# Performance work log

Measured on AMD Instinct MI355X. Metric: run time of the kernel, lower is better.

Reference implementation:

```python
import jax, jax.numpy as jnp
import numpy as np

S, F, H, A, B = 11, 650, 1024, 47, 4096
NEG = -1e9  # stand-in for -inf in masked_fill; softmax weight becomes exactly 0 numerically


def _layernorm(x, g, b):
    m = x.mean(-1, keepdims=True)
    v = ((x - m) ** 2).mean(-1, keepdims=True)
    return (x - m) / jnp.sqrt(v + 1e-5) * g + b


def setup_inputs() -> dict:
    key = jax.random.key(0)
    ks = jax.random.split(key, 16)

    def lin(k, fan_in, fan_out):
        kw, kb = jax.random.split(k)
        s = 1.0 / np.sqrt(fan_in)
        W = jax.random.uniform(kw, (fan_in, fan_out), minval=-s, maxval=s, dtype=jnp.float32)
        b = jax.random.uniform(kb, (fan_out,), minval=-s, maxval=s, dtype=jnp.float32)
        return W, b

    obs = jax.random.normal(ks[0], (B, S, F), dtype=jnp.float32)
    action_mask = jax.random.randint(ks[1], (B, 2, A), 0, 2).astype(jnp.int32)
    action_mask = action_mask.at[:, :, :8].set(1)  # guarantee legal actions per row
    u = jax.random.uniform(ks[2], (B, 2, A), minval=1e-6, maxval=1.0)
    gumbel = -jnp.log(-jnp.log(u))

    W0, b0 = lin(ks[3], S * F, H)
    W1, b1 = lin(ks[4], H, H)
    W2, b2 = lin(ks[5], H, H)
    Wp, bp = lin(ks[6], H, 2 * A)
    Wv, bv = lin(ks[7], H, 1)
    ones = jnp.ones((H,), jnp.float32)
    zeros = jnp.zeros((H,), jnp.float32)
    return {
        'obs': obs, 'action_mask': action_mask, 'gumbel': gumbel,
        'W0': W0, 'b0': b0, 'g0': ones, 'be0': zeros,
        'W1': W1, 'b1': b1, 'g1': ones, 'be1': zeros,
        'W2': W2, 'b2': b2, 'g2': ones, 'be2': zeros,
        'Wp': Wp, 'bp': bp, 'Wv': Wv, 'bv': bv,
    }


def _forward(obs, action_mask, gumbel, W0, b0, g0, be0, W1, b1, g1, be1, W2, b2, g2, be2, Wp, bp, Wv, bv):
    x = obs.reshape(obs.shape[0], -1)
    x = jax.nn.relu(_layernorm(x @ W0 + b0, g0, be0))
    x = jax.nn.relu(_layernorm(x @ W1 + b1, g1, be1))
    x = jax.nn.relu(_layernorm(x @ W2 + b2, g2, be2))  # dropout = eval-mode identity
    policy_logits = (x @ Wp + bp).reshape(-1, 2, A)
    value = (x @ Wv + bv)[:, 0]

    bsz = policy_logits.shape[0]
    rows = jnp.arange(bsz)
    ar = jnp.arange(A)

    # head 1: masked categorical via Gumbel-max
    l1 = jnp.where(action_mask[:, 0, :] == 0, NEG, policy_logits[:, 0, :])
    a1 = jnp.argmax(l1 + gumbel[:, 0, :], axis=-1)
    logp1 = jax.nn.log_softmax(l1, axis=-1)[rows, a1]

    # vectorized mutual-exclusivity mask update (replaces per-batch Python loop)
    m2 = action_mask[:, 1, :]
    oh = ar[None, :] == a1[:, None]
    c_switch = (a1 >= 1) & (a1 <= 6)
    m2 = jnp.where(c_switch[:, None] & oh, 0, m2)
    c_tera = (a1 > 26) & (a1 <= 46)
    rng = (ar >= 27) & (ar < 47)
    m2 = jnp.where(c_tera[:, None] & rng[None, :], 0, m2)
    c_zero = a1 == 0
    col0 = (ar == 0)[None, :]
    m2 = jnp.where(c_zero[:, None] & col0, 0, m2)
    empty = (m2.sum(-1) == 0) & c_zero
    m2 = jnp.where(empty[:, None] & col0, 1, m2)

    l2 = jnp.where(m2 == 0, NEG, policy_logits[:, 1, :])
    a2 = jnp.argmax(l2 + gumbel[:, 1, :], axis=-1)
    logp2 = jax.nn.log_softmax(l2, axis=-1)[rows, a2]

    sampled_actions = jnp.stack([a1, a2], axis=-1)
    policy_log_probs = jnp.stack([logp1, logp2], axis=-1)
    return policy_logits, policy_log_probs, sampled_actions, value


def reference(obs, action_mask, gumbel, W0, b0, g0, be0, W1, b1, g1, be1, W2, b2, g2, be2, Wp, bp, Wv, bv):
    return _forward(obs, action_mask, gumbel, W0, b0, g0, be0, W1, b1, g1, be1, W2, b2, g2, be2, Wp, bp, Wv, bv)
```

## Files before the change

kernel.cpp:

```cpp
#include <hip/hip_runtime.h>
#include <math.h>

#define BATCH 4096
#define HDIM  1024
#define KDIM0 7150
#define KP0   7168
#define KT0   224
#define KTH   32
#define NACT  47
#define NA2   94
#define NEGC  -1000000000.0f

#define LP_OFF  385024
#define ACT_OFF 393216
#define VAL_OFF 401408

typedef _Float16 half8_t  __attribute__((ext_vector_type(8)));
typedef _Float16 half4_t  __attribute__((ext_vector_type(4)));
typedef float    float4_t __attribute__((ext_vector_type(4)));

#define GLOAD16(gp, lp) __builtin_amdgcn_global_load_lds( \
    (__attribute__((address_space(1))) void*)(gp), \
    (__attribute__((address_space(3))) void*)(lp), 16, 0, 0)


__global__ __launch_bounds__(256) void wconv_frag_kernel(
    const float* __restrict__ W, _Float16* __restrict__ Wh,
    _Float16* __restrict__ Wl, int K, int KT)
{
  __shared__ float T[64][65];
  const int k0 = blockIdx.x * 64, n0 = blockIdx.y * 64, t = threadIdx.x;
#pragma unroll
  for (int p = 0; p < 16; ++p) {
    const int idx = p * 256 + t;
    const int r = idx >> 6, c = idx & 63;
    T[r][c] = (k0 + r < K) ? W[(size_t)(k0 + r) * HDIM + n0 + c] : 0.f;
  }
  __syncthreads();
#pragma unroll
  for (int ss = 0; ss < 2; ++ss) {
    const int s    = ss * 256 + t;
    const int tile = s >> 6;
    const int ktl  = tile >> 2, ntl = tile & 3;
    const int lane = s & 63;
    const int quad = lane >> 4, nr = lane & 15;
    half8_t h, l;
#pragma unroll
    for (int j = 0; j < 8; ++j) {
      const float v = T[ktl * 32 + quad * 8 + j][ntl * 16 + nr];
      const _Float16 hh = (_Float16)v;
      h[j] = hh;
      l[j] = (_Float16)((v - (float)hh) * 4096.f);
    }
    const size_t o = ((size_t)((n0 / 16 + ntl) * KT + (k0 / 32 + ktl)) * 64 + lane) * 8;
    *(half8_t*)(Wh + o) = h;
    *(half8_t*)(Wl + o) = l;
  }
}

__global__ __launch_bounds__(512, 4) void gemm_obs_kernel(
    const float* __restrict__ A,
    const _Float16* __restrict__ Wh, const _Float16* __restrict__ Wl,
    float* __restrict__ C, int ktsplit)
{
  __shared__ _Float16 As[2][2][8][512];
  __shared__ _Float16 Ws[2][2][8][512];
  const int f  = blockIdx.x + 8 * (blockIdx.y + 32 * blockIdx.z);
  const int nf = (f & 7) * 64 + (f >> 3);
  const int bx = nf & 7, by = (nf >> 3) & 31, bz = nf >> 8;

  const int t    = threadIdx.x;
  const int lane = t & 63;
  const int w    = t >> 6;
  const int nt0  = bx * 8;
  const int mt0  = by * 8;
  const int ktb  = bz * ktsplit;
  const int nit  = ktsplit >> 1;
  const int l15  = lane & 15, quad = lane >> 4;
  const int wmi  = (w >> 2) * 4;
  const int wni  = (w & 3) * 2;

  const float* aRow = A + (size_t)((mt0 + w) * 16 + l15) * KDIM0 + quad * 8;
  const _Float16* wS[2] = {
    Wh + (size_t)(nt0 + w) * KT0 * 512 + lane * 8,
    Wl + (size_t)(nt0 + w) * KT0 * 512 + lane * 8 };

  float4_t acc[4][2], accx[4][2];
#pragma unroll
  for (int i = 0; i < 4; ++i)
#pragma unroll
    for (int j = 0; j < 2; ++j) {
      acc[i][j]  = (float4_t){0.f, 0.f, 0.f, 0.f};
      accx[i][j] = (float4_t){0.f, 0.f, 0.f, 0.f};
    }

  for (int it = 0; it < nit; ++it) {
    const int ktg0 = ktb + it * 2;
    const size_t kb = (size_t)ktg0 * 512;

    float va[2][8];
#pragma unroll
    for (int k2 = 0; k2 < 2; ++k2) {
      const int kg = (ktg0 + k2) * 32 + quad * 8;
      const float* src = aRow + (size_t)(ktg0 + k2) * 32;
      if (kg + 8 <= KDIM0) {
#pragma unroll
        for (int c = 0; c < 4; ++c) {
          const float2 p = *(const float2*)(src + c * 2);
          va[k2][c * 2] = p.x; va[k2][c * 2 + 1] = p.y;
        }
      } else {
#pragma unroll
        for (int j = 0; j < 8; ++j)
          va[k2][j] = (kg + j < KDIM0) ? src[j] : 0.f;
      }
    }
#pragma unroll
    for (int k2 = 0; k2 < 2; ++k2)
#pragma unroll
      for (int pl = 0; pl < 2; ++pl)
        GLOAD16(wS[pl] + kb + k2 * 512, &Ws[k2][pl][w][0]);
#pragma unroll
    for (int k2 = 0; k2 < 2; ++k2) {
      half8_t h, l;
#pragma unroll
      for (int j = 0; j < 8; ++j) {
        const float v = va[k2][j];
        const _Float16 hh = (_Float16)v;
        h[j] = hh;
        l[j] = (_Float16)((v - (float)hh) * 4096.f);
      }
      *(half8_t*)&As[k2][0][w][lane * 8] = h;
      *(half8_t*)&As[k2][1][w][lane * 8] = l;
    }
    __syncthreads();
#pragma unroll
    for (int k2 = 0; k2 < 2; ++k2) {
      half8_t ah[4], al[4], wh[2], wl[2];
#pragma unroll
      for (int i = 0; i < 4; ++i) {
        ah[i] = *(const half8_t*)&As[k2][0][wmi + i][lane * 8];
        al[i] = *(const half8_t*)&As[k2][1][wmi + i][lane * 8];
      }
#pragma unroll
      for (int j = 0; j < 2; ++j) {
        wh[j] = *(const half8_t*)&Ws[k2][0][wni + j][lane * 8];
        wl[j] = *(const half8_t*)&Ws[k2][1][wni + j][lane * 8];
      }
#pragma unroll
      for (int i = 0; i < 4; ++i)
#pragma unroll
        for (int j = 0; j < 2; ++j) {
          acc[i][j]  = __builtin_amdgcn_mfma_f32_16x16x32_f16(ah[i], wh[j], acc[i][j], 0, 0, 0);
          accx[i][j] = __builtin_amdgcn_mfma_f32_16x16x32_f16(ah[i], wl[j], accx[i][j], 0, 0, 0);
          accx[i][j] = __builtin_amdgcn_mfma_f32_16x16x32_f16(al[i], wh[j], accx[i][j], 0, 0, 0);
        }
    }
    __syncthreads();
  }

  float* Cb = C + (size_t)bz * ((size_t)BATCH * HDIM);
  const float sc = 1.0f / 4096.0f;
#pragma unroll
  for (int i = 0; i < 4; ++i) {
    const int row0 = (mt0 + wmi + i) * 16 + quad * 4;
#pragma unroll
    for (int j = 0; j < 2; ++j) {
      const int col = (nt0 + wni + j) * 16 + l15;
      float* cp = Cb + (size_t)row0 * HDIM + col;
#pragma unroll
      for (int r = 0; r < 4; ++r)
        cp[(size_t)r * HDIM] = acc[i][j][r] + accx[i][j][r] * sc;
    }
  }
}

__global__ __launch_bounds__(512, 4) void gemm_frag2_kernel(
    const _Float16* __restrict__ Ah, const _Float16* __restrict__ Al,
    const _Float16* __restrict__ Wh, const _Float16* __restrict__ Wl,
    float* __restrict__ C, int KT, int ktsplit)
{
  __shared__ _Float16 As[2][2][8][512];
  __shared__ _Float16 Ws[2][2][8][512];
  const int f  = blockIdx.x + 8 * (blockIdx.y + 32 * blockIdx.z);
  const int nf = (f & 7) * 64 + (f >> 3);
  const int bx = nf & 7, by = (nf >> 3) & 31, bz = nf >> 8;

  const int t    = threadIdx.x;
  const int lane = t & 63;
  const int w    = t >> 6;
  const int nt0  = bx * 8;
  const int mt0  = by * 8;
  const int ktb  = bz * ktsplit;
  const int nit  = ktsplit >> 1;
  const int l15  = lane & 15, quad = lane >> 4;
  const int wmi  = (w >> 2) * 4;
  const int wni  = (w & 3) * 2;

  const _Float16* aS[2] = {
    Ah + (size_t)(mt0 + w) * KT * 512 + lane * 8,
    Al + (size_t)(mt0 + w) * KT * 512 + lane * 8 };
  const _Float16* wS[2] = {
    Wh + (size_t)(nt0 + w) * KT * 512 + lane * 8,
    Wl + (size_t)(nt0 + w) * KT * 512 + lane * 8 };

  float4_t acc[4][2], accx[4][2];
#pragma unroll
  for (int i = 0; i < 4; ++i)
#pragma unroll
    for (int j = 0; j < 2; ++j) {
      acc[i][j]  = (float4_t){0.f, 0.f, 0.f, 0.f};
      accx[i][j] = (float4_t){0.f, 0.f, 0.f, 0.f};
    }

  for (int it = 0; it < nit; ++it) {
    const size_t kb = (size_t)(ktb + it * 2) * 512;
#pragma unroll
    for (int k2 = 0; k2 < 2; ++k2)
#pragma unroll
      for (int pl = 0; pl < 2; ++pl) {
        GLOAD16(aS[pl] + kb + k2 * 512, &As[k2][pl][w][0]);
        GLOAD16(wS[pl] + kb + k2 * 512, &Ws[k2][pl][w][0]);
      }
    __syncthreads();
#pragma unroll
    for (int k2 = 0; k2 < 2; ++k2) {
      half8_t ah[4], al[4], wh[2], wl[2];
#pragma unroll
      for (int i = 0; i < 4; ++i) {
        ah[i] = *(const half8_t*)&As[k2][0][wmi + i][lane * 8];
        al[i] = *(const half8_t*)&As[k2][1][wmi + i][lane * 8];
      }
#pragma unroll
      for (int j = 0; j < 2; ++j) {
        wh[j] = *(const half8_t*)&Ws[k2][0][wni + j][lane * 8];
        wl[j] = *(const half8_t*)&Ws[k2][1][wni + j][lane * 8];
      }
#pragma unroll
      for (int i = 0; i < 4; ++i)
#pragma unroll
        for (int j = 0; j < 2; ++j) {
          acc[i][j]  = __builtin_amdgcn_mfma_f32_16x16x32_f16(ah[i], wh[j], acc[i][j], 0, 0, 0);
          accx[i][j] = __builtin_amdgcn_mfma_f32_16x16x32_f16(ah[i], wl[j], accx[i][j], 0, 0, 0);
          accx[i][j] = __builtin_amdgcn_mfma_f32_16x16x32_f16(al[i], wh[j], accx[i][j], 0, 0, 0);
        }
    }
    __syncthreads();
  }

  float* Cb = C + (size_t)bz * ((size_t)BATCH * HDIM);
  const float sc = 1.0f / 4096.0f;
#pragma unroll
  for (int i = 0; i < 4; ++i) {
    const int row0 = (mt0 + wmi + i) * 16 + quad * 4;
#pragma unroll
    for (int j = 0; j < 2; ++j) {
      const int col = (nt0 + wni + j) * 16 + l15;
      float* cp = Cb + (size_t)row0 * HDIM + col;
#pragma unroll
      for (int r = 0; r < 4; ++r)
        cp[(size_t)r * HDIM] = acc[i][j][r] + accx[i][j][r] * sc;
    }
  }
}

__global__ __launch_bounds__(1024) void ln_relu_f16_frag_kernel(
    const float* __restrict__ x0, const float* __restrict__ x1,
    const float* __restrict__ bias,
    const float* __restrict__ g, const float* __restrict__ be,
    _Float16* __restrict__ oh, _Float16* __restrict__ ol)
{
  const int t = threadIdx.x;
  const int w = t >> 6, lane = t & 63;
  const int mt = blockIdx.x;
  const float* xr0 = x0 + (size_t)(mt * 16 + w) * HDIM;
  const float* xr1 = x1 + (size_t)(mt * 16 + w) * HDIM;

  float4 v[4];
  float s = 0.f;
#pragma unroll
  for (int c = 0; c < 4; ++c) {
    const int k = c * 256 + lane * 4;
    const float4 a = *(const float4*)(xr0 + k);
    const float4 b = *(const float4*)(xr1 + k);
    const float4 bb = *(const float4*)(bias + k);
    v[c].x = a.x + b.x + bb.x; v[c].y = a.y + b.y + bb.y;
    v[c].z = a.z + b.z + bb.z; v[c].w = a.w + b.w + bb.w;
    s += (v[c].x + v[c].y) + (v[c].z + v[c].w);
  }
#pragma unroll
  for (int o = 32; o; o >>= 1) s += __shfl_xor(s, o, 64);
  const float mean = s * (1.0f / HDIM);

  float s2 = 0.f;
#pragma unroll
  for (int c = 0; c < 4; ++c) {
    v[c].x -= mean; v[c].y -= mean; v[c].z -= mean; v[c].w -= mean;
    s2 += (v[c].x * v[c].x + v[c].y * v[c].y) + (v[c].z * v[c].z + v[c].w * v[c].w);
  }
#pragma unroll
  for (int o = 32; o; o >>= 1) s2 += __shfl_xor(s2, o, 64);
  const float inv = 1.0f / sqrtf(s2 * (1.0f / HDIM) + 1e-5f);

  const int kt_b  = lane >> 3;
  const int quad  = (lane >> 1) & 3;
  const int jb    = (lane & 1) * 4;
#pragma unroll
  for (int c = 0; c < 4; ++c) {
    const int k = c * 256 + lane * 4;
    const float4 gg = *(const float4*)(g + k);
    const float4 ee = *(const float4*)(be + k);
    float r0 = fmaxf(fmaf(v[c].x * inv, gg.x, ee.x), 0.f);
    float r1 = fmaxf(fmaf(v[c].y * inv, gg.y, ee.y), 0.f);
    float r2 = fmaxf(fmaf(v[c].z * inv, gg.z, ee.z), 0.f);
    float r3 = fmaxf(fmaf(v[c].w * inv, gg.w, ee.w), 0.f);
    const _Float16 h0 = (_Float16)r0, h1 = (_Float16)r1, h2 = (_Float16)r2, h3 = (_Float16)r3;
    const half4_t hv = {h0, h1, h2, h3};
    const half4_t lv = {(_Float16)((r0 - (float)h0) * 4096.f),
                        (_Float16)((r1 - (float)h1) * 4096.f),
                        (_Float16)((r2 - (float)h2) * 4096.f),
                        (_Float16)((r3 - (float)h3) * 4096.f)};
    const int kt = c * 8 + kt_b;
    const size_t o = ((size_t)(mt * KTH + kt) * 64 + quad * 16 + w) * 8 + jb;
    *(half4_t*)(oh + o) = hv;
    *(half4_t*)(ol + o) = lv;
  }
}

__global__ __launch_bounds__(256) void pack_wcat_kernel(
    const float* __restrict__ Wp, const float* __restrict__ Wv,
    float* __restrict__ Wc)
{
  const int i = blockIdx.x * 256 + threadIdx.x;
  const int k = i / 96, c = i % 96;
  float v = 0.f;
  if (c < 94)       v = Wp[(size_t)k * 94 + c];
  else if (c == 94) v = Wv[k];
  Wc[i] = v;
}

__global__ __launch_bounds__(256) void head_fused_kernel(
    const float* __restrict__ x0, const float* __restrict__ x1,
    const float* __restrict__ b2, const float* __restrict__ g2,
    const float* __restrict__ be2,
    const float* __restrict__ Wc, const float* __restrict__ bp,
    const float* __restrict__ bv,
    const int* __restrict__ amask, const float* __restrict__ gum,
    float* __restrict__ out)
{
  __shared__ float Xs[8][1025];
  __shared__ float red[4][8][96];
  __shared__ float fl[8][96];
  __shared__ float rstat[16];
  const int t  = threadIdx.x;
  const int r0 = blockIdx.x * 8;
  const int wv = t >> 6, lane = t & 63;

#pragma unroll 4
  for (int i = 0; i < 32; ++i) {
    const int e = i * 256 + t;
    const int r = e >> 10, k = e & 1023;
    const size_t gi = (size_t)(r0 + r) * HDIM + k;
    Xs[r][k] = x0[gi] + x1[gi] + b2[k];
  }
  __syncthreads();

#pragma unroll
  for (int rr = 0; rr < 2; ++rr) {
    const int row = wv + rr * 4;
    float s = 0.f;
#pragma unroll
    for (int ii = 0; ii < 16; ++ii) s += Xs[row][lane + 64 * ii];
#pragma unroll
    for (int o = 32; o; o >>= 1) s += __shfl_xor(s, o, 64);
    const float mean = s * (1.0f / HDIM);
    float s2 = 0.f;
#pragma unroll
    for (int ii = 0; ii < 16; ++ii) {
      const float d = Xs[row][lane + 64 * ii] - mean;
      s2 += d * d;
    }
#pragma unroll
    for (int o = 32; o; o >>= 1) s2 += __shfl_xor(s2, o, 64);
    if (lane == 0) {
      rstat[row] = mean;
      rstat[8 + row] = 1.0f / sqrtf(s2 * (1.0f / HDIM) + 1e-5f);
    }
  }
  __syncthreads();

#pragma unroll 4
  for (int i = 0; i < 32; ++i) {
    const int e = i * 256 + t;
    const int r = e >> 10, k = e & 1023;
    Xs[r][k] = fmaxf(fmaf((Xs[r][k] - rstat[r]) * rstat[8 + r], g2[k], be2[k]), 0.f);
  }
  __syncthreads();

  const int tx = t & 15;
  const int ty = (t >> 4) & 3;
  const int kz = t >> 6;
  const int c0 = tx * 6;
  float acc[2][6] = {{0.f,0.f,0.f,0.f,0.f,0.f},{0.f,0.f,0.f,0.f,0.f,0.f}};
  const int kkend = kz * 256 + 256;
  for (int kk = kz * 256; kk < kkend; ++kk) {
    const float xa = Xs[ty * 2][kk];
    const float xb = Xs[ty * 2 + 1][kk];
    const float* wrow = Wc + (size_t)kk * 96 + c0;
    const float2 w01 = *(const float2*)(wrow);
    const float2 w23 = *(const float2*)(wrow + 2);
    const float2 w45 = *(const float2*)(wrow + 4);
    const float wvv[6] = {w01.x, w01.y, w23.x, w23.y, w45.x, w45.y};
#pragma unroll
    for (int j = 0; j < 6; ++j) {
      acc[0][j] = fmaf(xa, wvv[j], acc[0][j]);
      acc[1][j] = fmaf(xb, wvv[j], acc[1][j]);
    }
  }
#pragma unroll
  for (int r = 0; r < 2; ++r)
#pragma unroll
    for (int j = 0; j < 6; ++j) red[kz][ty * 2 + r][c0 + j] = acc[r][j];
  __syncthreads();

#pragma unroll
  for (int q = 0; q < 3; ++q) {
    const int e = t * 3 + q;
    const int row = e / 96, c = e % 96;
    const float sum = red[0][row][c] + red[1][row][c] + red[2][row][c] + red[3][row][c];
    if (c < 94) {
      const float vv = sum + bp[c];
      out[(size_t)(r0 + row) * NA2 + c] = vv;
      fl[row][c] = vv;
    } else if (c == 94) {
      out[VAL_OFF + r0 + row] = sum + bv[0];
    }
  }
  __syncthreads();

#pragma unroll
  for (int rr = 0; rr < 2; ++rr) {
    const int row = wv + rr * 4;
    const int b = r0 + row;
    const bool valid = lane < NACT;

    const float lg1 = valid ? fl[row][lane] : 0.f;
    const float lg2 = valid ? fl[row][NACT + lane] : 0.f;
    const int   mk1 = valid ? amask[(size_t)b * NA2 + lane] : 0;
    const int   mk2 = valid ? amask[(size_t)b * NA2 + NACT + lane] : 0;
    const float gu1 = valid ? gum[(size_t)b * NA2 + lane] : 0.f;
    const float gu2 = valid ? gum[(size_t)b * NA2 + NACT + lane] : 0.f;

    const float l1 = valid ? ((mk1 == 0) ? NEGC : lg1) : -INFINITY;
    float key = valid ? (l1 + gu1) : -INFINITY;
    int idx = lane;
#pragma unroll
    for (int o = 32; o; o >>= 1) {
      const float ok = __shfl_xor(key, o, 64);
      const int   oi = __shfl_xor(idx, o, 64);
      if (ok > key || (ok == key && oi < idx)) { key = ok; idx = oi; }
    }
    const int a1 = idx;

    float mx = l1;
#pragma unroll
    for (int o = 32; o; o >>= 1) mx = fmaxf(mx, __shfl_xor(mx, o, 64));
    float ex = valid ? expf(l1 - mx) : 0.f;
#pragma unroll
    for (int o = 32; o; o >>= 1) ex += __shfl_xor(ex, o, 64);
    const float logp1 = __shfl(l1, a1, 64) - (mx + logf(ex));

    int m2 = mk2;
    if (a1 >= 1 && a1 <= 6 && lane == a1) m2 = 0;
    if (a1 > 26 && a1 <= 46 && lane >= 27 && valid) m2 = 0;
    if (a1 == 0 && lane == 0) m2 = 0;
    int tot = m2;
#pragma unroll
    for (int o = 32; o; o >>= 1) tot += __shfl_xor(tot, o, 64);
    if (a1 == 0 && tot == 0 && lane == 0) m2 = 1;

    const float l2 = valid ? ((m2 == 0) ? NEGC : lg2) : -INFINITY;
    float key2 = valid ? (l2 + gu2) : -INFINITY;
    int idx2 = lane;
#pragma unroll
    for (int o = 32; o; o >>= 1) {
      const float ok = __shfl_xor(key2, o, 64);
      const int   oi = __shfl_xor(idx2, o, 64);
      if (ok > key2 || (ok == key2 && oi < idx2)) { key2 = ok; idx2 = oi; }
    }
    const int a2 = idx2;

    float mx2 = l2;
#pragma unroll
    for (int o = 32; o; o >>= 1) mx2 = fmaxf(mx2, __shfl_xor(mx2, o, 64));
    float ex2 = valid ? expf(l2 - mx2) : 0.f;
#pragma unroll
    for (int o = 32; o; o >>= 1) ex2 += __shfl_xor(ex2, o, 64);
    const float logp2 = __shfl(l2, a2, 64) - (mx2 + logf(ex2));

    if (lane == 0) {
      out[LP_OFF  + b * 2]     = logp1;
      out[LP_OFF  + b * 2 + 1] = logp2;
      out[ACT_OFF + b * 2]     = (float)a1;
      out[ACT_OFF + b * 2 + 1] = (float)a2;
    }
  }
}

extern "C" void kernel_launch(void* const* d_in, const int* in_sizes, int n_in,
                              void* d_out, int out_size, void* d_ws, size_t ws_size,
                              hipStream_t stream) {
  (void)in_sizes; (void)n_in; (void)out_size; (void)ws_size;
  const float* obs   = (const float*)d_in[0];
  const int*   amask = (const int*)  d_in[1];
  const float* gum   = (const float*)d_in[2];
  const float* W0    = (const float*)d_in[3];
  const float* b0    = (const float*)d_in[4];
  const float* g0    = (const float*)d_in[5];
  const float* be0   = (const float*)d_in[6];
  const float* W1    = (const float*)d_in[7];
  const float* b1    = (const float*)d_in[8];
  const float* g1    = (const float*)d_in[9];
  const float* be1   = (const float*)d_in[10];
  const float* W2    = (const float*)d_in[11];
  const float* b2    = (const float*)d_in[12];
  const float* g2    = (const float*)d_in[13];
  const float* be2   = (const float*)d_in[14];
  const float* Wp    = (const float*)d_in[15];
  const float* bp    = (const float*)d_in[16];
  const float* Wv    = (const float*)d_in[17];
  const float* bv    = (const float*)d_in[18];
  float* out = (float*)d_out;

  char* ws = (char*)d_ws;
  size_t off = 0;
  auto take = [&](size_t n) { char* p = ws + off; off += (n + 255) & ~(size_t)255; return p; };
  _Float16* w0h  = (_Float16*)take((size_t)HDIM * KP0 * 2);
  _Float16* w0l  = (_Float16*)take((size_t)HDIM * KP0 * 2);
  _Float16* w1h  = (_Float16*)take((size_t)HDIM * HDIM * 2);
  _Float16* w1l  = (_Float16*)take((size_t)HDIM * HDIM * 2);
  _Float16* w2h  = (_Float16*)take((size_t)HDIM * HDIM * 2);
  _Float16* w2l  = (_Float16*)take((size_t)HDIM * HDIM * 2);
  float*    xf   = (float*)   take((size_t)2 * BATCH * HDIM * 4);
  float*    wc   = (float*)   take((size_t)HDIM * 96 * 4);
  _Float16* xph  = w0h;
  _Float16* xpl  = w0l;
  float* xf1 = xf + (size_t)BATCH * HDIM;

  wconv_frag_kernel<<<dim3(KP0 / 64, 16), 256, 0, stream>>>(W0, w0h, w0l, KDIM0, KT0);
  wconv_frag_kernel<<<dim3(16, 16), 256, 0, stream>>>(W1, w1h, w1l, HDIM, KTH);
  wconv_frag_kernel<<<dim3(16, 16), 256, 0, stream>>>(W2, w2h, w2l, HDIM, KTH);
  pack_wcat_kernel<<<384, 256, 0, stream>>>(Wp, Wv, wc);

  gemm_obs_kernel<<<dim3(8, 32, 2), 512, 0, stream>>>(obs, w0h, w0l, xf, KT0 / 2);
  ln_relu_f16_frag_kernel<<<BATCH / 16, 1024, 0, stream>>>(xf, xf1, b0, g0, be0, xph, xpl);

  gemm_frag2_kernel<<<dim3(8, 32, 2), 512, 0, stream>>>(xph, xpl, w1h, w1l, xf, KTH, KTH / 2);
  ln_relu_f16_frag_kernel<<<BATCH / 16, 1024, 0, stream>>>(xf, xf1, b1, g1, be1, xph, xpl);

  gemm_frag2_kernel<<<dim3(8, 32, 2), 512, 0, stream>>>(xph, xpl, w2h, w2l, xf, KTH, KTH / 2);

  head_fused_kernel<<<BATCH / 8, 256, 0, stream>>>(
      xf, xf1, b2, g2, be2, wc, bp, bv, amask, gum, out);
}
```

Before: 568.6 us.

## Software-pipeline both split-K GEMM kernels with ping-pong LDS buffers

Both GEMM kernels now use the two LDS slots as a double buffer over single K-tiles. The next tile's weight (and activation) global-to-LDS loads are issued before the MFMA work on the current tile, and the obs kernel also prefetches fp32 activations into registers one step ahead. The goal is to hide global load latency behind matrix math instead of stalling on a barrier after every load phase. The trade-off is more register pressure. The tail handling assumes ktsplit is even, and it relies on global_load_lds completion being covered by __syncthreads.

```diff
diff --git a/kernel.cpp b/kernel.cpp
--- a/kernel.cpp
+++ b/kernel.cpp
@@ -75,15 +75,49 @@
   const int nt0  = bx * 8;
   const int mt0  = by * 8;
   const int ktb  = bz * ktsplit;
-  const int nit  = ktsplit >> 1;
+  const int nit  = ktsplit;
   const int l15  = lane & 15, quad = lane >> 4;
   const int wmi  = (w >> 2) * 4;
   const int wni  = (w & 3) * 2;
 
   const float* aRow = A + (size_t)((mt0 + w) * 16 + l15) * KDIM0 + quad * 8;
-  const _Float16* wS[2] = {
-    Wh + (size_t)(nt0 + w) * KT0 * 512 + lane * 8,
-    Wl + (size_t)(nt0 + w) * KT0 * 512 + lane * 8 };
+  const _Float16* wS0 = Wh + (size_t)(nt0 + w) * KT0 * 512 + lane * 8;
+  const _Float16* wS1 = Wl + (size_t)(nt0 + w) * KT0 * 512 + lane * 8;
+
+  struct AF8 { float v[8]; };
+  auto loadA = [&](int kt) {
+    AF8 r;
+    const int kg = kt * 32 + quad * 8;
+    const float* src = aRow + (size_t)kt * 32;
+    if (kg + 8 <= KDIM0) {
+#pragma unroll
+      for (int c = 0; c < 4; ++c) {
+        const float2 p = *(const float2*)(src + c * 2);
+        r.v[c * 2] = p.x; r.v[c * 2 + 1] = p.y;
+      }
+    } else {
+#pragma unroll
+      for (int j = 0; j < 8; ++j)
+        r.v[j] = (kg + j < KDIM0) ? src[j] : 0.f;
+    }
+    return r;
+  };
+  auto gw = [&](int kt, int buf) {
+    GLOAD16(wS0 + (size_t)kt * 512, &Ws[buf][0][w][0]);
+    GLOAD16(wS1 + (size_t)kt * 512, &Ws[buf][1][w][0]);
+  };
+  auto convst = [&](const AF8& a, int buf) {
+    half8_t h, l;
+#pragma unroll
+    for (int j = 0; j < 8; ++j) {
+      const float v = a.v[j];
+      const _Float16 hh = (_Float16)v;
+      h[j] = hh;
+      l[j] = (_Float16)((v - (float)hh) * 4096.f);
+    }
+    *(half8_t*)&As[buf][0][w][lane * 8] = h;
+    *(half8_t*)&As[buf][1][w][lane * 8] = l;
+  };
 
   float4_t acc[4][2], accx[4][2];
 #pragma unroll
@@ -94,68 +128,43 @@
       accx[i][j] = (float4_t){0.f, 0.f, 0.f, 0.f};
     }
 
-  for (int it = 0; it < nit; ++it) {
-    const int ktg0 = ktb + it * 2;
-    const size_t kb = (size_t)ktg0 * 512;
-
-    float va[2][8];
-#pragma unroll
-    for (int k2 = 0; k2 < 2; ++k2) {
-      const int kg = (ktg0 + k2) * 32 + quad * 8;
-      const float* src = aRow + (size_t)(ktg0 + k2) * 32;
-      if (kg + 8 <= KDIM0) {
-#pragma unroll
-        for (int c = 0; c < 4; ++c) {
-          const float2 p = *(const float2*)(src + c * 2);
-          va[k2][c * 2] = p.x; va[k2][c * 2 + 1] = p.y;
-        }
-      } else {
-#pragma unroll
-        for (int j = 0; j < 8; ++j)
-          va[k2][j] = (kg + j < KDIM0) ? src[j] : 0.f;
+  auto mm = [&](int buf) {
+    half8_t ah[4], al[4], wh[2], wl[2];
+#pragma unroll
+    for (int i = 0; i < 4; ++i) {
+      ah[i] = *(const half8_t*)&As[buf][0][wmi + i][lane * 8];
+      al[i] = *(const half8_t*)&As[buf][1][wmi + i][lane * 8];
+    }
+#pragma unroll
+    for (int j = 0; j < 2; ++j) {
+      wh[j] = *(const half8_t*)&Ws[buf][0][wni + j][lane * 8];
+      wl[j] = *(const half8_t*)&Ws[buf][1][wni + j][lane * 8];
+    }
+#pragma unroll
+    for (int i = 0; i < 4; ++i)
+#pragma unroll
+      for (int j = 0; j < 2; ++j) {
+        acc[i][j]  = __builtin_amdgcn_mfma_f32_16x16x32_f16(ah[i], wh[j], acc[i][j], 0, 0, 0);
+        accx[i][j] = __builtin_amdgcn_mfma_f32_16x16x32_f16(ah[i], wl[j], accx[i][j], 0, 0, 0);
+        accx[i][j] = __builtin_amdgcn_mfma_f32_16x16x32_f16(al[i], wh[j], accx[i][j], 0, 0, 0);
       }
-    }
-#pragma unroll
-    for (int k2 = 0; k2 < 2; ++k2)
-#pragma unroll
-      for (int pl = 0; pl < 2; ++pl)
-        GLOAD16(wS[pl] + kb + k2 * 512, &Ws[k2][pl][w][0]);
-#pragma unroll
-    for (int k2 = 0; k2 < 2; ++k2) {
-      half8_t h, l;
-#pragma unroll
-      for (int j = 0; j < 8; ++j) {
-        const float v = va[k2][j];
-        const _Float16 hh = (_Float16)v;
-        h[j] = hh;
-        l[j] = (_Float16)((v - (float)hh) * 4096.f);
-      }
-      *(half8_t*)&As[k2][0][w][lane * 8] = h;
-      *(half8_t*)&As[k2][1][w][lane * 8] = l;
-    }
+  };
+
+  AF8 vaE = loadA(ktb + 0);
+  AF8 vaO = loadA(ktb + 1);
+  gw(ktb + 0, 0);
+  convst(vaE, 0);
+  __syncthreads();
+
+  for (int it = 0; it < nit; it += 2) {
+    gw(ktb + it + 1, 1);
+    convst(vaO, 1);
+    if (it + 2 < nit) vaE = loadA(ktb + it + 2);
+    mm(0);
     __syncthreads();
-#pragma unroll
-    for (int k2 = 0; k2 < 2; ++k2) {
-      half8_t ah[4], al[4], wh[2], wl[2];
-#pragma unroll
-      for (int i = 0; i < 4; ++i) {
-        ah[i] = *(const half8_t*)&As[k2][0][wmi + i][lane * 8];
-        al[i] = *(const half8_t*)&As[k2][1][wmi + i][lane * 8];
-      }
-#pragma unroll
-      for (int j = 0; j < 2; ++j) {
-        wh[j] = *(const half8_t*)&Ws[k2][0][wni + j][lane * 8];
-        wl[j] = *(const half8_t*)&Ws[k2][1][wni + j][lane * 8];
-      }
-#pragma unroll
-      for (int i = 0; i < 4; ++i)
-#pragma unroll
-        for (int j = 0; j < 2; ++j) {
-          acc[i][j]  = __builtin_amdgcn_mfma_f32_16x16x32_f16(ah[i], wh[j], acc[i][j], 0, 0, 0);
-          accx[i][j] = __builtin_amdgcn_mfma_f32_16x16x32_f16(ah[i], wl[j], accx[i][j], 0, 0, 0);
-          accx[i][j] = __builtin_amdgcn_mfma_f32_16x16x32_f16(al[i], wh[j], accx[i][j], 0, 0, 0);
-        }
-    }
+    if (it + 2 < nit) { gw(ktb + it + 2, 0); convst(vaE, 0); }
+    if (it + 3 < nit) vaO = loadA(ktb + it + 3);
+    mm(1);
     __syncthreads();
   }
 
@@ -192,17 +201,22 @@
   const int nt0  = bx * 8;
   const int mt0  = by * 8;
   const int ktb  = bz * ktsplit;
-  const int nit  = ktsplit >> 1;
+  const int nit  = ktsplit;
   const int l15  = lane & 15, quad = lane >> 4;
   const int wmi  = (w >> 2) * 4;
   const int wni  = (w & 3) * 2;
 
-  const _Float16* aS[2] = {
-    Ah + (size_t)(mt0 + w) * KT * 512 + lane * 8,
-    Al + (size_t)(mt0 + w) * KT * 512 + lane * 8 };
-  const _Float16* wS[2] = {
-    Wh + (size_t)(nt0 + w) * KT * 512 + lane * 8,
-    Wl + (size_t)(nt0 + w) * KT * 512 + lane * 8 };
+  const _Float16* aS0 = Ah + (size_t)(mt0 + w) * KT * 512 + lane * 8;
+  const _Float16* aS1 = Al + (size_t)(mt0 + w) * KT * 512 + lane * 8;
+  const _Float16* wS0 = Wh + (size_t)(nt0 + w) * KT * 512 + lane * 8;
+  const _Float16* wS1 = Wl + (size_t)(nt0 + w) * KT * 512 + lane * 8;
+
+  auto st = [&](int kt, int buf) {
+    GLOAD16(aS0 + (size_t)kt * 512, &As[buf][0][w][0]);
+    GLOAD16(aS1 + (size_t)kt * 512, &As[buf][1][w][0]);
+    GLOAD16(wS0 + (size_t)kt * 512, &Ws[buf][0][w][0]);
+    GLOAD16(wS1 + (size_t)kt * 512, &Ws[buf][1][w][0]);
+  };
 
   float4_t acc[4][2], accx[4][2];
 #pragma unroll
@@ -213,38 +227,36 @@
       accx[i][j] = (float4_t){0.f, 0.f, 0.f, 0.f};
     }
 
-  for (int it = 0; it < nit; ++it) {
-    const size_t kb = (size_t)(ktb + it * 2) * 512;
-#pragma unroll
-    for (int k2 = 0; k2 < 2; ++k2)
-#pragma unroll
-      for (int pl = 0; pl < 2; ++pl) {
-        GLOAD16(aS[pl] + kb + k2 * 512, &As[k2][pl][w][0]);
-        GLOAD16(wS[pl] + kb + k2 * 512, &Ws[k2][pl][w][0]);
+  auto mm = [&](int buf) {
+    half8_t ah[4], al[4], wh[2], wl[2];
+#pragma unroll
+    for (int i = 0; i < 4; ++i) {
+      ah[i] = *(const half8_t*)&As[buf][0][wmi + i][lane * 8];
+      al[i] = *(const half8_t*)&As[buf][1][wmi + i][lane * 8];
+    }
+#pragma unroll
+    for (int j = 0; j < 2; ++j) {
+      wh[j] = *(const half8_t*)&Ws[buf][0][wni + j][lane * 8];
+      wl[j] = *(const half8_t*)&Ws[buf][1][wni + j][lane * 8];
+    }
+#pragma unroll
+    for (int i = 0; i < 4; ++i)
+#pragma unroll
+      for (int j = 0; j < 2; ++j) {
+        acc[i][j]  = __builtin_amdgcn_mfma_f32_16x16x32_f16(ah[i], wh[j], acc[i][j], 0, 0, 0);
+        accx[i][j] = __builtin_amdgcn_mfma_f32_16x16x32_f16(ah[i], wl[j], accx[i][j], 0, 0, 0);
+        accx[i][j] = __builtin_amdgcn_mfma_f32_16x16x32_f16(al[i], wh[j], accx[i][j], 0, 0, 0);
       }
+  };
+
+  st(ktb, 0);
+  __syncthreads();
+  for (int it = 0; it < nit; it += 2) {
+    st(ktb + it + 1, 1);
+    mm(0);
     __syncthreads();
-#pragma unroll
-    for (int k2 = 0; k2 < 2; ++k2) {
-      half8_t ah[4], al[4], wh[2], wl[2];
-#pragma unroll
-      for (int i = 0; i < 4; ++i) {
-        ah[i] = *(const half8_t*)&As[k2][0][wmi + i][lane * 8];
-        al[i] = *(const half8_t*)&As[k2][1][wmi + i][lane * 8];
-      }
-#pragma unroll
-      for (int j = 0; j < 2; ++j) {
-        wh[j] = *(const half8_t*)&Ws[k2][0][wni + j][lane * 8];
-        wl[j] = *(const half8_t*)&Ws[k2][1][wni + j][lane * 8];
-      }
-#pragma unroll
-      for (int i = 0; i < 4; ++i)
-#pragma unroll
-        for (int j = 0; j < 2; ++j) {
-          acc[i][j]  = __builtin_amdgcn_mfma_f32_16x16x32_f16(ah[i], wh[j], acc[i][j], 0, 0, 0);
-          accx[i][j] = __builtin_amdgcn_mfma_f32_16x16x32_f16(ah[i], wl[j], accx[i][j], 0, 0, 0);
-          accx[i][j] = __builtin_amdgcn_mfma_f32_16x16x32_f16(al[i], wh[j], accx[i][j], 0, 0, 0);
-        }
-    }
+    if (it + 2 < nit) st(ktb + it + 2, 0);
+    mm(1);
     __syncthreads();
   }
 
```

After: 530.7 us. -6.7%, faster.
